# Optimization experiments

Measured on AMD Instinct MI355X. Metric: run time of the kernel, lower is better.

## Reference

```python
import jax, jax.numpy as jnp
import numpy as np
import math

N_FREQS = 32
MARGIN = 0.1
CHOUT = 270
POS_DIM = 2 * N_FREQS ** 2  # 2048


def fourier_emb(positions):
    # positions: [..., 2] in [0, 1]
    width = 1.0 + 2.0 * MARGIN
    p = (positions + MARGIN) / width
    f = jnp.arange(N_FREQS, dtype=p.dtype)
    two_pi = 2.0 * math.pi
    # phase[..., i, j] = 2*pi*(x*i + y*j)  -> flatten to [..., F*F]
    phase = two_pi * (p[..., 0][..., None, None] * f[:, None]
                      + p[..., 1][..., None, None] * f[None, :])
    phase = phase.reshape(*phase.shape[:-2], N_FREQS * N_FREQS)
    return jnp.concatenate([jnp.sin(phase), jnp.cos(phase)], axis=-1)  # [..., 2F^2]


def setup_inputs() -> dict:
    key = jax.random.key(0)
    k1, k2, k3 = jax.random.split(key, 3)
    B, C, T = 32, 273, 3000
    brain_data = jax.random.normal(k1, (B, C, T), dtype=jnp.float32)
    channel_layout = jax.random.uniform(k2, (B, C, 2), dtype=jnp.float32)
    heads = jax.random.normal(k3, (CHOUT, POS_DIM), dtype=jnp.float32) / POS_DIM ** 0.5
    return {"brain_data": brain_data, "channel_layout": channel_layout, "heads": heads}


def reference(brain_data, channel_layout, heads):
    # Eval mode: all channels valid, no dropout mask, zero score offset.
    emb = fourier_emb(channel_layout)                      # [B, C, D]
    scores = jnp.einsum('bcd,od->boc', emb, heads)         # [B, O, C]
    weights = jax.nn.softmax(scores, axis=-1)              # softmax over channels
    out = jnp.einsum('bct,boc->bot', brain_data, weights)  # [B, O, T]
    return out
```

## Files before the change

### kernel.cpp

```cpp
#include <hip/hip_runtime.h>
#include <hip/hip_bf16.h>
#include <hip/hip_fp16.h>

#define NB 32
#define NC 273
#define NT 3000
#define NO 270
#define ND 2048
#define CP 288

typedef _Float16 f16x8 __attribute__((ext_vector_type(8)));
typedef float f32x4 __attribute__((ext_vector_type(4)));

#define S_OFF 55296000UL
#define W_OFF 64730880UL
#define H_OFF 69707520UL

__global__ void heads_cvt_kernel(const float* __restrict__ heads,
                                 _Float16* __restrict__ hh) {
  const size_t idx = ((size_t)blockIdx.x * 256 + threadIdx.x) * 8;
  const float4 a = *reinterpret_cast<const float4*>(heads + idx);
  const float4 c = *reinterpret_cast<const float4*>(heads + idx + 4);
  f16x8 v;
  v[0] = (_Float16)a.x; v[1] = (_Float16)a.y; v[2] = (_Float16)a.z; v[3] = (_Float16)a.w;
  v[4] = (_Float16)c.x; v[5] = (_Float16)c.y; v[6] = (_Float16)c.z; v[7] = (_Float16)c.w;
  *reinterpret_cast<f16x8*>(hh + idx) = v;
}

__global__ void scores_kernel(const _Float16* __restrict__ hh,
                              const float* __restrict__ layout,
                              float* __restrict__ scores) {
  __shared__ _Float16 As[64][72];
  __shared__ _Float16 Bs[64][72];
  const int gid = blockIdx.x;
  const int tid = threadIdx.x;
  const int b = gid / 25;
  const int rem = gid % 25;
  const int o0 = (rem / 5) * 64;
  const int c0 = (rem % 5) * 64;
  const int lane = tid & 63, w = tid >> 6;
  const int wm = (w >> 1) * 32, wn = (w & 1) * 32;
  const int ln = lane & 15, quad = lane >> 4;
  const int sr = tid >> 2;
  const int sk = (tid & 3) * 16;

  const int ch = c0 + sr;
  float px = 0.f, py = 0.f;
  if (ch < NC) {
    const float inv = 1.0f / 1.2f;
    const float* lp = layout + ((size_t)b * NC + ch) * 2;
    px = (lp[0] + 0.1f) * inv;
    py = (lp[1] + 0.1f) * inv;
  }

  f32x4 acc[2][2] = {};

  for (int k0 = 0; k0 < ND; k0 += 64) {
    {
      const int o = o0 + sr;
      uint4 u0 = {0, 0, 0, 0}, u1 = {0, 0, 0, 0};
      if (o < NO) {
        const uint4* p = reinterpret_cast<const uint4*>(hh + (size_t)o * ND + k0 + sk);
        u0 = p[0]; u1 = p[1];
      }
      *reinterpret_cast<uint4*>(&As[sr][sk]) = u0;
      *reinterpret_cast<uint4*>(&As[sr][sk + 8]) = u1;
    }
    {
      const int kg = k0 + sk;
      const int dd = kg & 1023;
      const float base = px * (float)(dd >> 5) + py * (float)(dd & 31)
                       + ((kg < 1024) ? 0.0f : 0.25f);
      f16x8 h0, h1;
#pragma unroll
      for (int s = 0; s < 8; ++s) {
        float ph = base + py * (float)s;
        ph -= floorf(ph);
        h0[s] = (_Float16)__builtin_amdgcn_sinf(ph);
      }
#pragma unroll
      for (int s = 0; s < 8; ++s) {
        float ph = base + py * (float)(s + 8);
        ph -= floorf(ph);
        h1[s] = (_Float16)__builtin_amdgcn_sinf(ph);
      }
      *reinterpret_cast<f16x8*>(&Bs[sr][sk]) = h0;
      *reinterpret_cast<f16x8*>(&Bs[sr][sk + 8]) = h1;
    }
    __syncthreads();
#pragma unroll
    for (int ks = 0; ks < 64; ks += 32) {
      const int kf = ks + quad * 8;
      const f16x8 a0 = *reinterpret_cast<const f16x8*>(&As[wm + ln][kf]);
      const f16x8 a1 = *reinterpret_cast<const f16x8*>(&As[wm + 16 + ln][kf]);
      const f16x8 b0 = *reinterpret_cast<const f16x8*>(&Bs[wn + ln][kf]);
      const f16x8 b1 = *reinterpret_cast<const f16x8*>(&Bs[wn + 16 + ln][kf]);
      acc[0][0] = __builtin_amdgcn_mfma_f32_16x16x32_f16(a0, b0, acc[0][0], 0, 0, 0);
      acc[0][1] = __builtin_amdgcn_mfma_f32_16x16x32_f16(a0, b1, acc[0][1], 0, 0, 0);
      acc[1][0] = __builtin_amdgcn_mfma_f32_16x16x32_f16(a1, b0, acc[1][0], 0, 0, 0);
      acc[1][1] = __builtin_amdgcn_mfma_f32_16x16x32_f16(a1, b1, acc[1][1], 0, 0, 0);
    }
    __syncthreads();
  }

  float* sB = scores + (size_t)b * NO * NC;
#pragma unroll
  for (int i = 0; i < 2; ++i) {
    const int ob = o0 + wm + 16 * i + quad * 4;
#pragma unroll
    for (int j = 0; j < 2; ++j) {
      const int cc = c0 + wn + 16 * j + ln;
      if (cc >= NC) continue;
#pragma unroll
      for (int r = 0; r < 4; ++r) {
        const int o = ob + r;
        if (o < NO) sB[(size_t)o * NC + cc] = acc[i][j][r];
      }
    }
  }
}

__global__ void softmax_kernel(const float* __restrict__ sc,
                               _Float16* __restrict__ wq) {
  const int row = blockIdx.x * 4 + (threadIdx.x >> 6);
  const int lane = threadIdx.x & 63;
  const float* p = sc + (size_t)row * NC;
  _Float16* q = wq + (size_t)row * CP;
  float v[5];
  float m = -3.0e38f;
#pragma unroll
  for (int k = 0; k < 5; ++k) {
    const int c = lane + k * 64;
    v[k] = (c < NC) ? p[c] : -3.0e38f;
    m = fmaxf(m, v[k]);
  }
#pragma unroll
  for (int off = 32; off > 0; off >>= 1) m = fmaxf(m, __shfl_xor(m, off));
  float s = 0.f;
#pragma unroll
  for (int k = 0; k < 5; ++k) {
    v[k] = expf(v[k] - m);
    s += v[k];
  }
#pragma unroll
  for (int off = 32; off > 0; off >>= 1) s += __shfl_xor(s, off);
  const float r = 1.0f / s;
#pragma unroll
  for (int k = 0; k < 5; ++k) {
    const int c = lane + k * 64;
    if (c < NC) q[c] = (_Float16)(v[k] * r);
    else if (c < CP) q[c] = (_Float16)0.f;
  }
}

__global__ __launch_bounds__(256, 2) void out_kernel(
    const _Float16* __restrict__ wq,
    const float* __restrict__ brain,
    float* __restrict__ out) {
  __shared__ float Bs[CP * 64];
  const int b = blockIdx.y;
  const int t0 = blockIdx.x * 64;
  const int tid = threadIdx.x;
  const int lane = tid & 63, w = tid >> 6;
  const int om = (w >> 1) * 32, tn = (w & 1) * 32;
  const int ln = lane & 15, quad = lane >> 4;

  const _Float16* Wb = wq + (size_t)b * NO * CP;

  auto load_a = [&](int s, f16x8 (&a)[10]) {
    const int kcol = s * 32 + quad * 8;
#pragma unroll
    for (int ot = 0; ot < 5; ++ot) {
      int r0 = ot * 64 + om + ln;      if (r0 > NO - 1) r0 = NO - 1;
      int r1 = ot * 64 + om + 16 + ln; if (r1 > NO - 1) r1 = NO - 1;
      a[2 * ot]     = *reinterpret_cast<const f16x8*>(Wb + (size_t)r0 * CP + kcol);
      a[2 * ot + 1] = *reinterpret_cast<const f16x8*>(Wb + (size_t)r1 * CP + kcol);
    }
  };

  f16x8 aE[10], aO[10];
  load_a(0, aE);

  {
    const int g16 = tid & 15;
    const int crow = tid >> 4;
    const float* gb = brain + (size_t)b * NC * NT + t0;
#pragma unroll
    for (int p = 0; p < 17; ++p) {
      const int c = p * 16 + crow;
      const int qc = (c >> 3) & 3;
      const float* gptr = gb + (size_t)c * NT + 4 * (g16 ^ (qc << 1));
      __builtin_amdgcn_global_load_lds(
          (const __attribute__((address_space(1))) void*)gptr,
          (__attribute__((address_space(3))) void*)(Bs + p * 1024 + w * 256),
          16, 0, 0);
    }
  }
  if (tid < 16) {
    const float* src = brain + ((size_t)b * NC + 272) * NT + t0;
    const int toff = 4 * (tid ^ 4);
    float4 v = {0.f, 0.f, 0.f, 0.f};
    if (t0 + toff + 3 < NT) {
      v = *reinterpret_cast<const float4*>(src + toff);
    } else {
      if (t0 + toff + 0 < NT) v.x = src[toff + 0];
      if (t0 + toff + 1 < NT) v.y = src[toff + 1];
      if (t0 + toff + 2 < NT) v.z = src[toff + 2];
    }
    *reinterpret_cast<float4*>(Bs + 272 * 64 + tid * 4) = v;
  }
  if (tid < 240) {
    const float4 z = {0.f, 0.f, 0.f, 0.f};
    *reinterpret_cast<float4*>(Bs + 273 * 64 + tid * 4) = z;
  }
  asm volatile("s_waitcnt vmcnt(0) lgkmcnt(0)" ::: "memory");
  __syncthreads();

  const int rc0 = (tn + ln) ^ (quad << 3);
  const int rc1 = (tn + 16 + ln) ^ (quad << 3);
  f32x4 acc[5][2][2] = {};

  auto do_mfma = [&](const f16x8 (&a)[10], f16x8 b0, f16x8 b1) {
#pragma unroll
    for (int ot = 0; ot < 5; ++ot) {
      acc[ot][0][0] = __builtin_amdgcn_mfma_f32_16x16x32_f16(a[2*ot],   b0, acc[ot][0][0], 0, 0, 0);
      acc[ot][0][1] = __builtin_amdgcn_mfma_f32_16x16x32_f16(a[2*ot],   b1, acc[ot][0][1], 0, 0, 0);
      acc[ot][1][0] = __builtin_amdgcn_mfma_f32_16x16x32_f16(a[2*ot+1], b0, acc[ot][1][0], 0, 0, 0);
      acc[ot][1][1] = __builtin_amdgcn_mfma_f32_16x16x32_f16(a[2*ot+1], b1, acc[ot][1][1], 0, 0, 0);
    }
  };

#pragma unroll
  for (int s = 0; s < 9; ++s) {
    if (s < 8) {
      if (((s + 1) & 1) == 0) load_a(s + 1, aE); else load_a(s + 1, aO);
    }
    f16x8 b0, b1;
#pragma unroll
    for (int j = 0; j < 8; ++j) {
      const int c = s * 32 + quad * 8 + j;
      b0[j] = (_Float16)Bs[c * 64 + rc0];
      b1[j] = (_Float16)Bs[c * 64 + rc1];
    }
    if ((s & 1) == 0) do_mfma(aE, b0, b1); else do_mfma(aO, b0, b1);
  }

  float* oB = out + (size_t)b * NO * NT;
#pragma unroll
  for (int ot = 0; ot < 5; ++ot) {
#pragma unroll
    for (int i = 0; i < 2; ++i) {
      const int ob = ot * 64 + om + 16 * i + quad * 4;
#pragma unroll
      for (int j = 0; j < 2; ++j) {
        const int t = t0 + tn + 16 * j + ln;
        if (t >= NT) continue;
#pragma unroll
        for (int r = 0; r < 4; ++r) {
          const int o = ob + r;
          if (o < NO) oB[(size_t)o * NT + t] = acc[ot][i][j][r];
        }
      }
    }
  }
}

extern "C" void kernel_launch(void* const* d_in, const int* in_sizes, int n_in,
                              void* d_out, int out_size, void* d_ws, size_t ws_size,
                              hipStream_t stream) {
  const float* brain = (const float*)d_in[0];
  const float* layout = (const float*)d_in[1];
  const float* heads = (const float*)d_in[2];
  for (int i = 0; i < n_in; ++i) {
    if (in_sizes[i] == NB * NC * NT) brain = (const float*)d_in[i];
    else if (in_sizes[i] == NB * NC * 2) layout = (const float*)d_in[i];
    else if (in_sizes[i] == NO * ND) heads = (const float*)d_in[i];
  }
  float* out = (float*)d_out;

  float* scores = (float*)((char*)d_ws + S_OFF);
  _Float16* wq = (_Float16*)((char*)d_ws + W_OFF);
  _Float16* hh = (_Float16*)((char*)d_ws + H_OFF);

  heads_cvt_kernel<<<NO, 256, 0, stream>>>(heads, hh);
  scores_kernel<<<800, 256, 0, stream>>>(hh, layout, scores);
  softmax_kernel<<<(NB * NO) / 4, 256, 0, stream>>>(scores, wq);
  out_kernel<<<dim3(47, NB), 256, 0, stream>>>(wq, brain, out);
}
```

Measured before the change: 286.3 us.

## Retile out_kernel to 192-wide time tiles with fp16 LDS staging

Restructures the output GEMM so each 512-thread block covers a 192-wide time tile across all 270 outputs. The brain tile is converted to fp16 once when it is written to shared memory, so the inner loop no longer converts per element. The block index is remapped to interleave batches, and the launch drops from 47x32 blocks to 512. The larger tiles are meant to reuse the weight fragments across more time columns and cut redundant A loads. In exchange, the async global-to-LDS copy is replaced by register-staged loads, and per-thread register pressure rises with 30 accumulators.

```diff
diff --git a/kernel.cpp b/kernel.cpp
--- a/kernel.cpp
+++ b/kernel.cpp
@@ -15,6 +15,13 @@
 #define S_OFF 55296000UL
 #define W_OFF 64730880UL
 #define H_OFF 69707520UL
+
+__device__ __forceinline__ unsigned short f2h_bits(float f) {
+  _Float16 h = (_Float16)f;
+  unsigned short u;
+  __builtin_memcpy(&u, &h, 2);
+  return u;
+}
 
 __global__ void heads_cvt_kernel(const float* __restrict__ heads,
                                  _Float16* __restrict__ hh) {
@@ -153,113 +160,108 @@
   }
 }
 
-__global__ __launch_bounds__(256, 2) void out_kernel(
+#define TS 192
+
+__global__ __launch_bounds__(512, 2) void out_kernel(
     const _Float16* __restrict__ wq,
     const float* __restrict__ brain,
     float* __restrict__ out) {
-  __shared__ float Bs[CP * 64];
-  const int b = blockIdx.y;
-  const int t0 = blockIdx.x * 64;
+  __shared__ _Float16 SB[CP * TS];
+  const int flat = blockIdx.x;
+  const int b = (flat & 7) * 4 + ((flat >> 3) & 3);
+  const int t0 = (flat >> 5) * TS;
   const int tid = threadIdx.x;
-  const int lane = tid & 63, w = tid >> 6;
-  const int om = (w >> 1) * 32, tn = (w & 1) * 32;
+
+  {
+    float4 vbuf[26];
+#pragma unroll
+    for (int p = 0; p < 26; ++p) {
+      const int idx = p * 512 + tid;
+      const int c = idx / 48, g = idx % 48;
+      float4 v = {0.f, 0.f, 0.f, 0.f};
+      if (c < NC) {
+        int toff = t0 + 4 * g;
+        if (toff > NT - 4) toff = NT - 4;
+        v = *reinterpret_cast<const float4*>(brain + ((size_t)b * NC + c) * NT + toff);
+      }
+      vbuf[p] = v;
+    }
+    if (tid < 360) {
+      const uint4 z = {0, 0, 0, 0};
+      *reinterpret_cast<uint4*>(&SB[NC * TS + tid * 8]) = z;
+    }
+#pragma unroll
+    for (int p = 0; p < 26; ++p) {
+      const int idx = p * 512 + tid;
+      const int c = idx / 48, g = idx % 48;
+      if (c < NC) {
+        const int qc = (c >> 3) & 3;
+        const int h = c * TS + ((4 * g) ^ (qc << 4));
+        uint2 u;
+        u.x = (unsigned)f2h_bits(vbuf[p].x) | ((unsigned)f2h_bits(vbuf[p].y) << 16);
+        u.y = (unsigned)f2h_bits(vbuf[p].z) | ((unsigned)f2h_bits(vbuf[p].w) << 16);
+        *reinterpret_cast<uint2*>(&SB[h]) = u;
+      }
+    }
+  }
+  __syncthreads();
+
+  const int w = tid >> 6, lane = tid & 63;
   const int ln = lane & 15, quad = lane >> 4;
-
+  const int wm = (w >> 1) * 80;
+  const int wn = (w & 1) * 96;
   const _Float16* Wb = wq + (size_t)b * NO * CP;
 
-  auto load_a = [&](int s, f16x8 (&a)[10]) {
-    const int kcol = s * 32 + quad * 8;
-#pragma unroll
-    for (int ot = 0; ot < 5; ++ot) {
-      int r0 = ot * 64 + om + ln;      if (r0 > NO - 1) r0 = NO - 1;
-      int r1 = ot * 64 + om + 16 + ln; if (r1 > NO - 1) r1 = NO - 1;
-      a[2 * ot]     = *reinterpret_cast<const f16x8*>(Wb + (size_t)r0 * CP + kcol);
-      a[2 * ot + 1] = *reinterpret_cast<const f16x8*>(Wb + (size_t)r1 * CP + kcol);
+  f32x4 acc[5][6] = {};
+  f16x8 afA[5], afB[5];
+
+  auto load_af = [&](int s, f16x8 (&af)[5]) {
+    const int col = s * 32 + quad * 8;
+#pragma unroll
+    for (int i = 0; i < 5; ++i) {
+      int o = wm + i * 16 + ln;
+      if (o > NO - 1) o = NO - 1;
+      af[i] = *reinterpret_cast<const f16x8*>(Wb + (size_t)o * CP + col);
     }
   };
 
-  f16x8 aE[10], aO[10];
-  load_a(0, aE);
-
-  {
-    const int g16 = tid & 15;
-    const int crow = tid >> 4;
-    const float* gb = brain + (size_t)b * NC * NT + t0;
-#pragma unroll
-    for (int p = 0; p < 17; ++p) {
-      const int c = p * 16 + crow;
-      const int qc = (c >> 3) & 3;
-      const float* gptr = gb + (size_t)c * NT + 4 * (g16 ^ (qc << 1));
-      __builtin_amdgcn_global_load_lds(
-          (const __attribute__((address_space(1))) void*)gptr,
-          (__attribute__((address_space(3))) void*)(Bs + p * 1024 + w * 256),
-          16, 0, 0);
-    }
-  }
-  if (tid < 16) {
-    const float* src = brain + ((size_t)b * NC + 272) * NT + t0;
-    const int toff = 4 * (tid ^ 4);
-    float4 v = {0.f, 0.f, 0.f, 0.f};
-    if (t0 + toff + 3 < NT) {
-      v = *reinterpret_cast<const float4*>(src + toff);
-    } else {
-      if (t0 + toff + 0 < NT) v.x = src[toff + 0];
-      if (t0 + toff + 1 < NT) v.y = src[toff + 1];
-      if (t0 + toff + 2 < NT) v.z = src[toff + 2];
-    }
-    *reinterpret_cast<float4*>(Bs + 272 * 64 + tid * 4) = v;
-  }
-  if (tid < 240) {
-    const float4 z = {0.f, 0.f, 0.f, 0.f};
-    *reinterpret_cast<float4*>(Bs + 273 * 64 + tid * 4) = z;
-  }
-  asm volatile("s_waitcnt vmcnt(0) lgkmcnt(0)" ::: "memory");
-  __syncthreads();
-
-  const int rc0 = (tn + ln) ^ (quad << 3);
-  const int rc1 = (tn + 16 + ln) ^ (quad << 3);
-  f32x4 acc[5][2][2] = {};
-
-  auto do_mfma = [&](const f16x8 (&a)[10], f16x8 b0, f16x8 b1) {
-#pragma unroll
-    for (int ot = 0; ot < 5; ++ot) {
-      acc[ot][0][0] = __builtin_amdgcn_mfma_f32_16x16x32_f16(a[2*ot],   b0, acc[ot][0][0], 0, 0, 0);
-      acc[ot][0][1] = __builtin_amdgcn_mfma_f32_16x16x32_f16(a[2*ot],   b1, acc[ot][0][1], 0, 0, 0);
-      acc[ot][1][0] = __builtin_amdgcn_mfma_f32_16x16x32_f16(a[2*ot+1], b0, acc[ot][1][0], 0, 0, 0);
-      acc[ot][1][1] = __builtin_amdgcn_mfma_f32_16x16x32_f16(a[2*ot+1], b1, acc[ot][1][1], 0, 0, 0);
-    }
-  };
-
+  load_af(0, afA);
 #pragma unroll
   for (int s = 0; s < 9; ++s) {
     if (s < 8) {
-      if (((s + 1) & 1) == 0) load_a(s + 1, aE); else load_a(s + 1, aO);
-    }
-    f16x8 b0, b1;
-#pragma unroll
-    for (int j = 0; j < 8; ++j) {
-      const int c = s * 32 + quad * 8 + j;
-      b0[j] = (_Float16)Bs[c * 64 + rc0];
-      b1[j] = (_Float16)Bs[c * 64 + rc1];
-    }
-    if ((s & 1) == 0) do_mfma(aE, b0, b1); else do_mfma(aO, b0, b1);
+      if (s & 1) load_af(s + 1, afA); else load_af(s + 1, afB);
+    }
+    f16x8 bf[6];
+#pragma unroll
+    for (int nf = 0; nf < 6; ++nf) {
+      const int tsw = (wn + nf * 16 + ln) ^ (quad << 4);
+#pragma unroll
+      for (int j = 0; j < 8; ++j) {
+        const int c = s * 32 + quad * 8 + j;
+        bf[nf][j] = SB[c * TS + tsw];
+      }
+    }
+    const f16x8(&af)[5] = (s & 1) ? afB : afA;
+#pragma unroll
+    for (int i = 0; i < 5; ++i) {
+#pragma unroll
+      for (int nf = 0; nf < 6; ++nf) {
+        acc[i][nf] = __builtin_amdgcn_mfma_f32_16x16x32_f16(af[i], bf[nf], acc[i][nf], 0, 0, 0);
+      }
+    }
   }
 
   float* oB = out + (size_t)b * NO * NT;
 #pragma unroll
-  for (int ot = 0; ot < 5; ++ot) {
-#pragma unroll
-    for (int i = 0; i < 2; ++i) {
-      const int ob = ot * 64 + om + 16 * i + quad * 4;
-#pragma unroll
-      for (int j = 0; j < 2; ++j) {
-        const int t = t0 + tn + 16 * j + ln;
-        if (t >= NT) continue;
-#pragma unroll
-        for (int r = 0; r < 4; ++r) {
-          const int o = ob + r;
-          if (o < NO) oB[(size_t)o * NT + t] = acc[ot][i][j][r];
-        }
+  for (int i = 0; i < 5; ++i) {
+#pragma unroll
+    for (int nf = 0; nf < 6; ++nf) {
+      const int t = t0 + wn + nf * 16 + ln;
+      if (t >= NT) continue;
+#pragma unroll
+      for (int r = 0; r < 4; ++r) {
+        const int o = wm + i * 16 + quad * 4 + r;
+        if (o < NO) oB[(size_t)o * NT + t] = acc[i][nf][r];
       }
     }
   }
@@ -285,5 +287,5 @@
   heads_cvt_kernel<<<NO, 256, 0, stream>>>(heads, hh);
   scores_kernel<<<800, 256, 0, stream>>>(hh, layout, scores);
   softmax_kernel<<<(NB * NO) / 4, 256, 0, stream>>>(scores, wq);
-  out_kernel<<<dim3(47, NB), 256, 0, stream>>>(wq, brain, out);
-}
+  out_kernel<<<512, 512, 0, stream>>>(wq, brain, out);
+}
```

New measurement: 266.7 us. 1.07x faster.
